# Optimization experiments

Measured on AMD Instinct MI355X. Metric: run time of the kernel, lower is better.

Reference implementation:

```python
import jax, jax.numpy as jnp
import numpy as np

N_NODES = 4194304  # 2**22
LEVELS = 10
COARSE = 8192
RANK = 2
NNZ = 8388608


def _interp_linear(u, N):
    """torch F.interpolate(mode='linear', align_corners=False) along axis 1. u: (B,M,R) -> (B,N,R)."""
    M = u.shape[1]
    pos = (jnp.arange(N, dtype=jnp.float32) + 0.5) * (M / N) - 0.5
    pos = jnp.clip(pos, 0.0, M - 1)
    i0 = jnp.floor(pos).astype(jnp.int32)
    i1 = jnp.minimum(i0 + 1, M - 1)
    w = (pos - i0.astype(jnp.float32))[None, :, None]
    return u[:, i0] * (1.0 - w) + u[:, i1] * w


def _apply_hodlr(diag, u_factors, v_factors, x):
    B, N, _ = x.shape
    y = diag * x
    L = u_factors.shape[0]
    for lvl in range(L):
        num_splits = 2 ** (lvl + 1)
        bs = N // num_splits
        if bs == 0:
            continue
        uc, vc = u_factors[lvl], v_factors[lvl]
        u_full = _interp_linear(uc, N) if uc.shape[1] != N else uc
        v_full = _interp_linear(vc, N) if vc.shape[1] != N else vc
        P = num_splits // 2
        valid = P * 2 * bs
        xv = x[:, :valid].reshape(B, P, 2, bs, 1)
        uv = u_full[:, :valid].reshape(B, P, 2, bs, -1)
        vv = v_full[:, :valid].reshape(B, P, 2, bs, -1)
        xL, xR = xv[:, :, 0], xv[:, :, 1]
        uL, uR = uv[:, :, 0], uv[:, :, 1]
        vL, vR = vv[:, :, 0], vv[:, :, 1]
        xRp = jnp.einsum('bpkr,bpko->bpro', vR, xR)  # (B,P,R,1)
        xLp = jnp.einsum('bpkr,bpko->bpro', vL, xL)
        yL = jnp.einsum('bpkr,bpro->bpko', uL, xRp)  # (B,P,bs,1)
        yR = jnp.einsum('bpkr,bpro->bpko', uR, xLp)
        upd = jnp.stack([yL, yR], axis=2).reshape(B, valid, 1)
        if valid < N:
            upd = jnp.pad(upd, ((0, 0), (0, N - valid), (0, 0)))
        y = y + upd
    return y


def setup_inputs() -> dict:
    key = jax.random.key(0)
    ks = jax.random.split(key, 6)
    diag = jax.random.uniform(ks[0], (1, N_NODES, 1), dtype=jnp.float32)
    u_factors = jax.random.normal(ks[1], (LEVELS, 1, COARSE, RANK), dtype=jnp.float32)
    v_factors = jax.random.normal(ks[2], (LEVELS, 1, COARSE, RANK), dtype=jnp.float32)
    A_values = jax.random.normal(ks[3], (NNZ,), dtype=jnp.float32)
    z = jax.random.normal(ks[4], (1, N_NODES, 1), dtype=jnp.float32)
    A_indices = jax.random.randint(ks[5], (2, NNZ), 0, N_NODES, dtype=jnp.int64) if jax.config.jax_enable_x64 else jax.random.randint(ks[5], (2, NNZ), 0, N_NODES, dtype=jnp.int32)
    return {"diag": diag, "u_factors": u_factors, "v_factors": v_factors,
            "A_values": A_values, "z": z, "A_indices": A_indices, "num_nodes": N_NODES}


def reference(diag, u_factors, v_factors, A_values, z, A_indices, num_nodes):
    N = num_nodes
    w = _apply_hodlr(diag, u_factors, v_factors, z)          # (1,N,1)
    w_flat = w.reshape(N)
    rows, cols = A_indices[0], A_indices[1]
    y_flat = jax.ops.segment_sum(A_values * w_flat[cols], rows, num_segments=N)
    y = y_flat.reshape(1, N, 1)
    loss = jnp.mean((y - z) ** 2)
    return loss
```

## Files before the change

kernel.cpp:

```cpp
#include <hip/hip_runtime.h>

#define N_NODES   4194304
#define LEVELS    10
#define COARSE    8192
#define NNZ_E     8388608
#define NCHUNK    16384
#define NBUCK     256
#define BROWS     16384
#define BSH       14
#define HBLOCKS   2048
#define EPB       4096

typedef int          v4i __attribute__((ext_vector_type(4)));
typedef float        v4f __attribute__((ext_vector_type(4)));
typedef unsigned int v4u __attribute__((ext_vector_type(4)));

static __device__ __forceinline__ unsigned short f2bf(float x) {
    unsigned u = __float_as_uint(x);
    return (unsigned short)((u + 0x7FFFu + ((u >> 16) & 1u)) >> 16);
}
static __device__ __forceinline__ float bf2f(unsigned short h) {
    return __uint_as_float((unsigned)h << 16);
}
static __device__ __forceinline__ unsigned pack18(int lrow, float p) {
    unsigned u = __float_as_uint(p);
    return ((unsigned)lrow << 18) | (((u + 0x2000u) >> 14) & 0x3FFFFu);
}

__global__ __launch_bounds__(256) void kA_moments(const float* __restrict__ z,
                                                  float2* __restrict__ M,
                                                  float* __restrict__ S,
                                                  float* __restrict__ out) {
    if (blockIdx.x == 0) {
        for (int i = threadIdx.x; i < 2046 * 2; i += 256) S[i] = 0.f;
        if (threadIdx.x == 0) out[0] = 0.f;
    }
    int lane = threadIdx.x & 63;
    int wave = threadIdx.x >> 6;
    int chunk = blockIdx.x * 4 + wave;
    int base = chunk * 256 + lane * 4;
    float4 zv = *(const float4*)(z + base);
    float a0 = 0.f, a1 = 0.f;
    const float* zp = (const float*)&zv;
#pragma unroll
    for (int j = 0; j < 4; ++j) {
        float p = ((float)(base + j) + 0.5f) * (1.0f / 512.0f) - 0.5f;
        p = fminf(fmaxf(p, 0.0f), (float)(COARSE - 1));
        float f = p - floorf(p);
        a0 += zp[j] * (1.0f - f);
        a1 += zp[j] * f;
    }
#pragma unroll
    for (int off = 32; off >= 1; off >>= 1) {
        a0 += __shfl_xor(a0, off, 64);
        a1 += __shfl_xor(a1, off, 64);
    }
    if (lane == 0) M[chunk] = make_float2(a0, a1);
}

__global__ __launch_bounds__(1024) void kB_ssum(const float2* __restrict__ M,
                                                const float* __restrict__ V,
                                                float* __restrict__ S) {
    int lvl = blockIdx.x >> 3;
    int slice = blockIdx.x & 7;
    int t = threadIdx.x;
    const float2* Vl = (const float2*)(V + lvl * COARSE * 2);
    float s0 = 0.f, s1 = 0.f;
    int c0 = slice * 2048 + t * 2;
#pragma unroll
    for (int cc = 0; cc < 2; ++cc) {
        int c = c0 + cc;
        float2 m = M[c];
        int k = (c > 0) ? ((c - 1) >> 1) : 0;
        int kp = min(k + 1, COARSE - 1);
        float2 vk = Vl[k], vkp = Vl[kp];
        s0 += vk.x * m.x + vkp.x * m.y;
        s1 += vk.y * m.x + vkp.y * m.y;
    }
    int tpg_sh = 12 - lvl;
    int gw = min(1 << tpg_sh, 64);
    for (int sh = gw >> 1; sh >= 1; sh >>= 1) {
        s0 += __shfl_xor(s0, sh, 64);
        s1 += __shfl_xor(s1, sh, 64);
    }
    if ((t & (gw - 1)) == 0) {
        int b = c0 >> (13 - lvl);
        int soff = (2 << lvl) - 2;
        unsafeAtomicAdd(&S[(soff + b) * 2 + 0], s0);
        unsafeAtomicAdd(&S[(soff + b) * 2 + 1], s1);
    }
}

__global__ __launch_bounds__(256) void kC_g(const float* __restrict__ S,
                                            const float* __restrict__ U,
                                            float2* __restrict__ G) {
    int c = blockIdx.x * 256 + threadIdx.x;
    int k = (c > 0) ? ((c - 1) >> 1) : 0;
    int kp = min(k + 1, COARSE - 1);
    float g0 = 0.f, g1 = 0.f;
#pragma unroll
    for (int lvl = 0; lvl < LEVELS; ++lvl) {
        int sib = (c >> (13 - lvl)) ^ 1;
        int soff = (2 << lvl) - 2;
        float2 s = ((const float2*)S)[soff + sib];
        const float2* Ul = (const float2*)(U + lvl * COARSE * 2);
        float2 uk = Ul[k], ukp = Ul[kp];
        g0 += uk.x * s.x + uk.y * s.y;
        g1 += ukp.x * s.x + ukp.y * s.y;
    }
    G[c] = make_float2(g0, g1);
}

__global__ __launch_bounds__(256) void kW(const float* __restrict__ diag,
                                          const float* __restrict__ z,
                                          const float2* __restrict__ G,
                                          unsigned short* __restrict__ wb) {
    int tid = blockIdx.x * 256 + threadIdx.x;
    int base = tid * 4;
    float2 g = G[base >> 8];
    v4f d4 = __builtin_nontemporal_load((const v4f*)(diag + base));
    v4f z4 = __builtin_nontemporal_load((const v4f*)(z + base));
    const float* dp = (const float*)&d4;
    const float* zp = (const float*)&z4;
    ushort4 h4;
    unsigned short* hp = (unsigned short*)&h4;
#pragma unroll
    for (int j = 0; j < 4; ++j) {
        float p = ((float)(base + j) + 0.5f) * (1.0f / 512.0f) - 0.5f;
        p = fminf(fmaxf(p, 0.0f), (float)(COARSE - 1));
        float f = p - floorf(p);
        hp[j] = f2bf(dp[j] * zp[j] + (g.x + f * (g.y - g.x)));
    }
    *(ushort4*)(wb + base) = h4;
}

__global__ __launch_bounds__(256) void kHist(const int* __restrict__ rows,
                                             unsigned int* __restrict__ blockOff) {
    __shared__ unsigned int h[NBUCK];
    int blk = blockIdx.x, t = threadIdx.x;
    h[t] = 0u;
    __syncthreads();
    int base = blk * EPB;
#pragma unroll
    for (int it = 0; it < 4; ++it) {
        int e = base + it * 1024 + t * 4;
        v4i r = __builtin_nontemporal_load((const v4i*)(rows + e));
        atomicAdd(&h[r.x >> BSH], 1u);
        atomicAdd(&h[r.y >> BSH], 1u);
        atomicAdd(&h[r.z >> BSH], 1u);
        atomicAdd(&h[r.w >> BSH], 1u);
    }
    __syncthreads();
    blockOff[t * HBLOCKS + blk] = h[t];
}

__global__ __launch_bounds__(256) void kScan1(unsigned int* __restrict__ blockOff,
                                              unsigned int* __restrict__ total) {
    int b = blockIdx.x, t = threadIdx.x;
    unsigned int* p = blockOff + b * HBLOCKS;
    v4u a = *(const v4u*)(p + t * 8);
    v4u c = *(const v4u*)(p + t * 8 + 4);
    unsigned int s = a.x + a.y + a.z + a.w + c.x + c.y + c.z + c.w;
    unsigned int incl = s;
#pragma unroll
    for (int off = 1; off < 64; off <<= 1) {
        unsigned int n = __shfl_up(incl, off, 64);
        if ((t & 63) >= off) incl += n;
    }
    __shared__ unsigned int wsum[4], wbase[4];
    if ((t & 63) == 63) wsum[t >> 6] = incl;
    __syncthreads();
    if (t == 0) {
        unsigned int acc = 0;
        for (int i = 0; i < 4; ++i) { wbase[i] = acc; acc += wsum[i]; }
        total[b] = acc;
    }
    __syncthreads();
    unsigned int excl = wbase[t >> 6] + incl - s;
    v4u e0, e1;
    e0.x = excl;        e0.y = e0.x + a.x; e0.z = e0.y + a.y; e0.w = e0.z + a.z;
    e1.x = e0.w + a.w;  e1.y = e1.x + c.x; e1.z = e1.y + c.y; e1.w = e1.z + c.z;
    *(v4u*)(p + t * 8) = e0;
    *(v4u*)(p + t * 8 + 4) = e1;
}

__global__ __launch_bounds__(256) void kBinScatter(const int* __restrict__ rows,
                                                   const int* __restrict__ cols,
                                                   const float* __restrict__ vals,
                                                   const unsigned short* __restrict__ wb,
                                                   const unsigned int* __restrict__ blockOff,
                                                   const unsigned int* __restrict__ total,
                                                   unsigned int* __restrict__ packed) {
    __shared__ unsigned int ctr[NBUCK];
    __shared__ unsigned int wsum[4], wbase[4];
    int blk = blockIdx.x, t = threadIdx.x;
    unsigned int tv = total[t];
    unsigned int incl = tv;
#pragma unroll
    for (int off = 1; off < 64; off <<= 1) {
        unsigned int n = __shfl_up(incl, off, 64);
        if ((t & 63) >= off) incl += n;
    }
    if ((t & 63) == 63) wsum[t >> 6] = incl;
    __syncthreads();
    if (t == 0) {
        unsigned int a = 0;
        for (int i = 0; i < 4; ++i) { wbase[i] = a; a += wsum[i]; }
    }
    __syncthreads();
    ctr[t] = (wbase[t >> 6] + incl - tv) + blockOff[t * HBLOCKS + blk];
    __syncthreads();

    int base = blk * EPB;
    v4i r[4], c[4];
    v4f v[4];
#pragma unroll
    for (int j = 0; j < 4; ++j) {
        int e = base + j * 1024 + t * 4;
        r[j] = __builtin_nontemporal_load((const v4i*)(rows + e));
        c[j] = __builtin_nontemporal_load((const v4i*)(cols + e));
        v[j] = __builtin_nontemporal_load((const v4f*)(vals + e));
    }
    unsigned short wv[16];
#pragma unroll
    for (int j = 0; j < 4; ++j) {
        const int* cp = (const int*)&c[j];
        wv[j * 4 + 0] = wb[cp[0]];
        wv[j * 4 + 1] = wb[cp[1]];
        wv[j * 4 + 2] = wb[cp[2]];
        wv[j * 4 + 3] = wb[cp[3]];
    }
#pragma unroll
    for (int j = 0; j < 4; ++j) {
        const int* rp = (const int*)&r[j];
        const float* vp = (const float*)&v[j];
#pragma unroll
        for (int k = 0; k < 4; ++k) {
            int row = rp[k];
            float p = vp[k] * bf2f(wv[j * 4 + k]);
            unsigned int pos = atomicAdd(&ctr[row >> BSH], 1u);
            packed[pos] = pack18(row & (BROWS - 1), p);
        }
    }
}

__global__ __launch_bounds__(1024) void kBucketAccum(const unsigned int* __restrict__ packed,
                                                     const unsigned int* __restrict__ total,
                                                     const float* __restrict__ z,
                                                     float* __restrict__ out) {
    __shared__ float acc[BROWS];
    __shared__ unsigned int sb, sn;
    __shared__ unsigned int wsum[4], wbase[4];
    __shared__ float red[16];
    int b = blockIdx.x, t = threadIdx.x;

    unsigned int tv = 0, incl = 0;
    if (t < 256) {
        tv = total[t];
        incl = tv;
#pragma unroll
        for (int off = 1; off < 64; off <<= 1) {
            unsigned int n = __shfl_up(incl, off, 64);
            if ((t & 63) >= off) incl += n;
        }
        if ((t & 63) == 63) wsum[t >> 6] = incl;
    }
    __syncthreads();
    if (t == 0) {
        unsigned int a = 0;
        for (int i = 0; i < 4; ++i) { wbase[i] = a; a += wsum[i]; }
    }
    __syncthreads();
    if (t < 256 && t == b) { sb = wbase[t >> 6] + incl - tv; sn = tv; }
    for (int i = t; i < BROWS / 4; i += 1024) ((float4*)acc)[i] = make_float4(0.f, 0.f, 0.f, 0.f);
    __syncthreads();

    unsigned int s0 = sb, n = sn;
    for (unsigned int i = t; i < n; i += 1024) {
        unsigned int e = __builtin_nontemporal_load(packed + s0 + i);
        atomicAdd(&acc[e >> 18], __uint_as_float((e & 0x3FFFFu) << 14));
    }
    __syncthreads();

    float part = 0.f;
    int gbase = b * BROWS;
    for (int i = t; i < BROWS; i += 1024) {
        float d = acc[i] - z[gbase + i];
        part += d * d;
    }
#pragma unroll
    for (int off = 32; off >= 1; off >>= 1) part += __shfl_xor(part, off, 64);
    if ((t & 63) == 0) red[t >> 6] = part;
    __syncthreads();
    if (t == 0) {
        float s = 0.f;
        for (int i = 0; i < 16; ++i) s += red[i];
        unsafeAtomicAdd(out, s * (1.0f / (float)N_NODES));
    }
}

extern "C" void kernel_launch(void* const* d_in, const int* in_sizes, int n_in,
                              void* d_out, int out_size, void* d_ws, size_t ws_size,
                              hipStream_t stream) {
    const float* diag  = (const float*)d_in[0];
    const float* U     = (const float*)d_in[1];
    const float* V     = (const float*)d_in[2];
    const float* Avals = (const float*)d_in[3];
    const float* z     = (const float*)d_in[4];
    const int*   Aidx  = (const int*)d_in[5];
    const int* rows = Aidx;
    const int* cols = Aidx + NNZ_E;

    char* ws = (char*)d_ws;
    size_t off = 0;
    unsigned short* wb = (unsigned short*)(ws + off); off += (size_t)N_NODES * 2;
    unsigned int* packed = (unsigned int*)(ws + off); off += (size_t)NNZ_E * 4;
    unsigned int* blockOff = (unsigned int*)(ws + off); off += (size_t)NBUCK * HBLOCKS * 4;
    unsigned int* total    = (unsigned int*)(ws + off); off += NBUCK * 4;
    float2* M  = (float2*)(ws + off); off += NCHUNK * 8;
    float*  S  = (float*)(ws + off);  off += 2046 * 2 * 4;
    float2* G  = (float2*)(ws + off); off += NCHUNK * 8;

    kA_moments<<<NCHUNK / 4, 256, 0, stream>>>(z, M, S, (float*)d_out);
    kB_ssum<<<LEVELS * 8, 1024, 0, stream>>>(M, V, S);
    kC_g<<<NCHUNK / 256, 256, 0, stream>>>(S, U, G);
    kW<<<N_NODES / 1024, 256, 0, stream>>>(diag, z, G, wb);

    kHist<<<HBLOCKS, 256, 0, stream>>>(rows, blockOff);
    kScan1<<<NBUCK, 256, 0, stream>>>(blockOff, total);
    kBinScatter<<<HBLOCKS, 256, 0, stream>>>(rows, cols, Avals, wb, blockOff, total, packed);
    kBucketAccum<<<NBUCK, 1024, 0, stream>>>(packed, total, z, (float*)d_out);
}
```

Before: 341.6 us.

## Two-pass column-then-row binning with LDS-resident w slices and fused launches

Replaces the random bf16 gather of w by first binning edges by column bucket, so each block of kD4 holds a 16K-entry fp32 w slice in shared memory and gathers from LDS. Kernel D4 then rebins products by row bucket into packed entries for the final accumulate. Independent stages (moments/histograms, ssum/scans, w compute/column scatter) are merged into fewer launches via blockIdx ranges. It removes scattered global gathers and launch overhead at the cost of an extra 8-byte-per-edge pass and more global traffic.

```diff
diff --git a/kernel.cpp b/kernel.cpp
--- a/kernel.cpp
+++ b/kernel.cpp
@@ -1,15 +1,16 @@
 #include <hip/hip_runtime.h>
 
-#define N_NODES   4194304
-#define LEVELS    10
-#define COARSE    8192
-#define NNZ_E     8388608
-#define NCHUNK    16384
-#define NBUCK     256
-#define BROWS     16384
-#define BSH       14
-#define HBLOCKS   2048
-#define EPB       4096
+#define N_NODES 4194304
+#define LEVELS  10
+#define COARSE  8192
+#define NNZ_E   8388608
+#define NCHUNK  16384
+#define NB      256
+#define CB_SZ   16384
+#define RB_SZ   16384
+#define HB      2048
+#define EPB     4096
+#define KMAX    34
 
 typedef int          v4i __attribute__((ext_vector_type(4)));
 typedef float        v4f __attribute__((ext_vector_type(4)));
@@ -22,269 +23,357 @@
 static __device__ __forceinline__ float bf2f(unsigned short h) {
     return __uint_as_float((unsigned)h << 16);
 }
-static __device__ __forceinline__ unsigned pack18(int lrow, float p) {
-    unsigned u = __float_as_uint(p);
-    return ((unsigned)lrow << 18) | (((u + 0x2000u) >> 14) & 0x3FFFFu);
-}
-
-__global__ __launch_bounds__(256) void kA_moments(const float* __restrict__ z,
-                                                  float2* __restrict__ M,
-                                                  float* __restrict__ S,
-                                                  float* __restrict__ out) {
-    if (blockIdx.x == 0) {
-        for (int i = threadIdx.x; i < 2046 * 2; i += 256) S[i] = 0.f;
-        if (threadIdx.x == 0) out[0] = 0.f;
-    }
-    int lane = threadIdx.x & 63;
-    int wave = threadIdx.x >> 6;
-    int chunk = blockIdx.x * 4 + wave;
-    int base = chunk * 256 + lane * 4;
-    float4 zv = *(const float4*)(z + base);
-    float a0 = 0.f, a1 = 0.f;
-    const float* zp = (const float*)&zv;
-#pragma unroll
-    for (int j = 0; j < 4; ++j) {
-        float p = ((float)(base + j) + 0.5f) * (1.0f / 512.0f) - 0.5f;
-        p = fminf(fmaxf(p, 0.0f), (float)(COARSE - 1));
-        float f = p - floorf(p);
-        a0 += zp[j] * (1.0f - f);
-        a1 += zp[j] * f;
-    }
-#pragma unroll
-    for (int off = 32; off >= 1; off >>= 1) {
-        a0 += __shfl_xor(a0, off, 64);
-        a1 += __shfl_xor(a1, off, 64);
-    }
-    if (lane == 0) M[chunk] = make_float2(a0, a1);
-}
-
-__global__ __launch_bounds__(1024) void kB_ssum(const float2* __restrict__ M,
-                                                const float* __restrict__ V,
-                                                float* __restrict__ S) {
-    int lvl = blockIdx.x >> 3;
-    int slice = blockIdx.x & 7;
-    int t = threadIdx.x;
-    const float2* Vl = (const float2*)(V + lvl * COARSE * 2);
-    float s0 = 0.f, s1 = 0.f;
-    int c0 = slice * 2048 + t * 2;
-#pragma unroll
-    for (int cc = 0; cc < 2; ++cc) {
-        int c = c0 + cc;
-        float2 m = M[c];
+static __device__ __forceinline__ unsigned f18(float p) {
+    return ((__float_as_uint(p) + 0x2000u) >> 14) & 0x3FFFFu;
+}
+
+__global__ __launch_bounds__(256) void kD1(const float* __restrict__ z,
+                                           float2* __restrict__ M,
+                                           float* __restrict__ S,
+                                           float* __restrict__ out,
+                                           const int* __restrict__ rows,
+                                           const int* __restrict__ cols,
+                                           unsigned* __restrict__ colBO,
+                                           unsigned* __restrict__ rowBC) {
+    int b = blockIdx.x, t = threadIdx.x;
+    if (b < 4096) {
+        if (b == 0) {
+            for (int i = t; i < 2046 * 2; i += 256) S[i] = 0.f;
+            if (t == 0) out[0] = 0.f;
+        }
+        int lane = t & 63, wave = t >> 6;
+        int chunk = b * 4 + wave;
+        int base = chunk * 256 + lane * 4;
+        float4 zv = *(const float4*)(z + base);
+        float a0 = 0.f, a1 = 0.f;
+        const float* zp = (const float*)&zv;
+#pragma unroll
+        for (int j = 0; j < 4; ++j) {
+            float p = ((float)(base + j) + 0.5f) * (1.0f / 512.0f) - 0.5f;
+            p = fminf(fmaxf(p, 0.0f), (float)(COARSE - 1));
+            float f = p - floorf(p);
+            a0 += zp[j] * (1.0f - f);
+            a1 += zp[j] * f;
+        }
+#pragma unroll
+        for (int off = 32; off >= 1; off >>= 1) {
+            a0 += __shfl_xor(a0, off, 64);
+            a1 += __shfl_xor(a1, off, 64);
+        }
+        if (lane == 0) M[chunk] = make_float2(a0, a1);
+    } else {
+        __shared__ unsigned hc[NB], hr[NB];
+        int blk = b - 4096;
+        hc[t] = 0u; hr[t] = 0u;
+        __syncthreads();
+        int base = blk * EPB;
+#pragma unroll
+        for (int it = 0; it < 4; ++it) {
+            int e = base + it * 1024 + t * 4;
+            v4i r = *(const v4i*)(rows + e);
+            v4i c = *(const v4i*)(cols + e);
+            atomicAdd(&hr[r.x >> 14], 1u); atomicAdd(&hr[r.y >> 14], 1u);
+            atomicAdd(&hr[r.z >> 14], 1u); atomicAdd(&hr[r.w >> 14], 1u);
+            atomicAdd(&hc[c.x >> 14], 1u); atomicAdd(&hc[c.y >> 14], 1u);
+            atomicAdd(&hc[c.z >> 14], 1u); atomicAdd(&hc[c.w >> 14], 1u);
+        }
+        __syncthreads();
+        colBO[t * HB + blk] = hc[t];
+        rowBC[t * HB + blk] = hr[t];
+    }
+}
+
+__global__ __launch_bounds__(1024) void kD2(const float2* __restrict__ M,
+                                            const float* __restrict__ V,
+                                            float* __restrict__ S,
+                                            unsigned* __restrict__ colBO,
+                                            unsigned* __restrict__ colTotal,
+                                            const unsigned* __restrict__ rowBC,
+                                            unsigned* __restrict__ rowTotal) {
+    int b = blockIdx.x, t = threadIdx.x;
+    if (b < 80) {
+        int lvl = b >> 3, slice = b & 7;
+        const float2* Vl = (const float2*)(V + lvl * COARSE * 2);
+        float s0 = 0.f, s1 = 0.f;
+        int c0 = slice * 2048 + t * 2;
+#pragma unroll
+        for (int cc = 0; cc < 2; ++cc) {
+            int c = c0 + cc;
+            float2 m = M[c];
+            int k = (c > 0) ? ((c - 1) >> 1) : 0;
+            int kp = min(k + 1, COARSE - 1);
+            float2 vk = Vl[k], vkp = Vl[kp];
+            s0 += vk.x * m.x + vkp.x * m.y;
+            s1 += vk.y * m.x + vkp.y * m.y;
+        }
+        int gw = min(1 << (12 - lvl), 64);
+        for (int sh = gw >> 1; sh >= 1; sh >>= 1) {
+            s0 += __shfl_xor(s0, sh, 64);
+            s1 += __shfl_xor(s1, sh, 64);
+        }
+        if ((t & (gw - 1)) == 0) {
+            int bb = c0 >> (13 - lvl);
+            int soff = (2 << lvl) - 2;
+            unsafeAtomicAdd(&S[(soff + bb) * 2 + 0], s0);
+            unsafeAtomicAdd(&S[(soff + bb) * 2 + 1], s1);
+        }
+    } else if (b < 336) {
+        int bb = b - 80;
+        __shared__ unsigned wsum[4], wbase[4];
+        if (t < 256) {
+            unsigned* p = colBO + bb * HB;
+            v4u a = *(const v4u*)(p + t * 8);
+            v4u c = *(const v4u*)(p + t * 8 + 4);
+            unsigned s = a.x + a.y + a.z + a.w + c.x + c.y + c.z + c.w;
+            unsigned incl = s;
+#pragma unroll
+            for (int off = 1; off < 64; off <<= 1) {
+                unsigned n = __shfl_up(incl, off, 64);
+                if ((t & 63) >= off) incl += n;
+            }
+            if ((t & 63) == 63) wsum[t >> 6] = incl;
+            __syncthreads();
+            if (t == 0) {
+                unsigned acc = 0;
+                for (int i = 0; i < 4; ++i) { wbase[i] = acc; acc += wsum[i]; }
+                colTotal[bb] = acc;
+            }
+            __syncthreads();
+            unsigned excl = wbase[t >> 6] + incl - s;
+            v4u e0, e1;
+            e0.x = excl;       e0.y = e0.x + a.x; e0.z = e0.y + a.y; e0.w = e0.z + a.z;
+            e1.x = e0.w + a.w; e1.y = e1.x + c.x; e1.z = e1.y + c.y; e1.w = e1.z + c.z;
+            *(v4u*)(p + t * 8) = e0;
+            *(v4u*)(p + t * 8 + 4) = e1;
+        } else {
+            __syncthreads();
+            __syncthreads();
+        }
+    } else {
+        int bb = b - 336;
+        __shared__ unsigned red[8];
+        unsigned s = 0;
+        if (t < 512) {
+            v4u vv = *(const v4u*)(rowBC + bb * HB + t * 4);
+            s = vv.x + vv.y + vv.z + vv.w;
+        }
+#pragma unroll
+        for (int off = 32; off >= 1; off >>= 1) s += __shfl_xor(s, off, 64);
+        if (t < 512 && (t & 63) == 0) red[t >> 6] = s;
+        __syncthreads();
+        if (t == 0) {
+            unsigned tot = 0;
+            for (int i = 0; i < 8; ++i) tot += red[i];
+            rowTotal[bb] = tot;
+        }
+    }
+}
+
+__global__ __launch_bounds__(256) void kD3(const float* __restrict__ diag,
+                                           const float* __restrict__ z,
+                                           const float* __restrict__ S,
+                                           const float* __restrict__ U,
+                                           float* __restrict__ w,
+                                           const int* __restrict__ rows,
+                                           const int* __restrict__ cols,
+                                           const float* __restrict__ vals,
+                                           const unsigned* __restrict__ colTotal,
+                                           const unsigned* __restrict__ colBO,
+                                           uint2* __restrict__ colBinned,
+                                           const unsigned* __restrict__ rowTotal,
+                                           unsigned* __restrict__ rowBase,
+                                           unsigned* __restrict__ rowCtr) {
+    int b = blockIdx.x, t = threadIdx.x;
+    if (b < 4096) {
+        int tid = b * 256 + t;
+        int base = tid * 4;
+        int c = base >> 8;
         int k = (c > 0) ? ((c - 1) >> 1) : 0;
         int kp = min(k + 1, COARSE - 1);
-        float2 vk = Vl[k], vkp = Vl[kp];
-        s0 += vk.x * m.x + vkp.x * m.y;
-        s1 += vk.y * m.x + vkp.y * m.y;
-    }
-    int tpg_sh = 12 - lvl;
-    int gw = min(1 << tpg_sh, 64);
-    for (int sh = gw >> 1; sh >= 1; sh >>= 1) {
-        s0 += __shfl_xor(s0, sh, 64);
-        s1 += __shfl_xor(s1, sh, 64);
-    }
-    if ((t & (gw - 1)) == 0) {
-        int b = c0 >> (13 - lvl);
-        int soff = (2 << lvl) - 2;
-        unsafeAtomicAdd(&S[(soff + b) * 2 + 0], s0);
-        unsafeAtomicAdd(&S[(soff + b) * 2 + 1], s1);
-    }
-}
-
-__global__ __launch_bounds__(256) void kC_g(const float* __restrict__ S,
-                                            const float* __restrict__ U,
-                                            float2* __restrict__ G) {
-    int c = blockIdx.x * 256 + threadIdx.x;
-    int k = (c > 0) ? ((c - 1) >> 1) : 0;
-    int kp = min(k + 1, COARSE - 1);
-    float g0 = 0.f, g1 = 0.f;
-#pragma unroll
-    for (int lvl = 0; lvl < LEVELS; ++lvl) {
-        int sib = (c >> (13 - lvl)) ^ 1;
-        int soff = (2 << lvl) - 2;
-        float2 s = ((const float2*)S)[soff + sib];
-        const float2* Ul = (const float2*)(U + lvl * COARSE * 2);
-        float2 uk = Ul[k], ukp = Ul[kp];
-        g0 += uk.x * s.x + uk.y * s.y;
-        g1 += ukp.x * s.x + ukp.y * s.y;
-    }
-    G[c] = make_float2(g0, g1);
-}
-
-__global__ __launch_bounds__(256) void kW(const float* __restrict__ diag,
-                                          const float* __restrict__ z,
-                                          const float2* __restrict__ G,
-                                          unsigned short* __restrict__ wb) {
-    int tid = blockIdx.x * 256 + threadIdx.x;
-    int base = tid * 4;
-    float2 g = G[base >> 8];
-    v4f d4 = __builtin_nontemporal_load((const v4f*)(diag + base));
-    v4f z4 = __builtin_nontemporal_load((const v4f*)(z + base));
-    const float* dp = (const float*)&d4;
-    const float* zp = (const float*)&z4;
-    ushort4 h4;
-    unsigned short* hp = (unsigned short*)&h4;
-#pragma unroll
-    for (int j = 0; j < 4; ++j) {
-        float p = ((float)(base + j) + 0.5f) * (1.0f / 512.0f) - 0.5f;
-        p = fminf(fmaxf(p, 0.0f), (float)(COARSE - 1));
-        float f = p - floorf(p);
-        hp[j] = f2bf(dp[j] * zp[j] + (g.x + f * (g.y - g.x)));
-    }
-    *(ushort4*)(wb + base) = h4;
-}
-
-__global__ __launch_bounds__(256) void kHist(const int* __restrict__ rows,
-                                             unsigned int* __restrict__ blockOff) {
-    __shared__ unsigned int h[NBUCK];
-    int blk = blockIdx.x, t = threadIdx.x;
-    h[t] = 0u;
-    __syncthreads();
-    int base = blk * EPB;
-#pragma unroll
-    for (int it = 0; it < 4; ++it) {
-        int e = base + it * 1024 + t * 4;
-        v4i r = __builtin_nontemporal_load((const v4i*)(rows + e));
-        atomicAdd(&h[r.x >> BSH], 1u);
-        atomicAdd(&h[r.y >> BSH], 1u);
-        atomicAdd(&h[r.z >> BSH], 1u);
-        atomicAdd(&h[r.w >> BSH], 1u);
-    }
-    __syncthreads();
-    blockOff[t * HBLOCKS + blk] = h[t];
-}
-
-__global__ __launch_bounds__(256) void kScan1(unsigned int* __restrict__ blockOff,
-                                              unsigned int* __restrict__ total) {
+        float g0 = 0.f, g1 = 0.f;
+#pragma unroll
+        for (int lvl = 0; lvl < LEVELS; ++lvl) {
+            int sib = (c >> (13 - lvl)) ^ 1;
+            int soff = (2 << lvl) - 2;
+            float2 s2 = ((const float2*)S)[soff + sib];
+            const float2* Ul = (const float2*)(U + lvl * COARSE * 2);
+            float2 uk = Ul[k], ukp = Ul[kp];
+            g0 += uk.x * s2.x + uk.y * s2.y;
+            g1 += ukp.x * s2.x + ukp.y * s2.y;
+        }
+        float4 d4 = *(const float4*)(diag + base);
+        float4 z4 = *(const float4*)(z + base);
+        const float* dp = (const float*)&d4;
+        const float* zp = (const float*)&z4;
+        float4 w4;
+        float* wp = (float*)&w4;
+#pragma unroll
+        for (int j = 0; j < 4; ++j) {
+            float p = ((float)(base + j) + 0.5f) * (1.0f / 512.0f) - 0.5f;
+            p = fminf(fmaxf(p, 0.0f), (float)(COARSE - 1));
+            float f = p - floorf(p);
+            wp[j] = dp[j] * zp[j] + (g0 + f * (g1 - g0));
+        }
+        *(float4*)(w + base) = w4;
+    } else if (b < 6144) {
+        int blk = b - 4096;
+        __shared__ unsigned ctr[NB];
+        __shared__ unsigned wsum[4], wbase[4];
+        unsigned tv = colTotal[t];
+        unsigned incl = tv;
+#pragma unroll
+        for (int off = 1; off < 64; off <<= 1) {
+            unsigned n = __shfl_up(incl, off, 64);
+            if ((t & 63) >= off) incl += n;
+        }
+        if ((t & 63) == 63) wsum[t >> 6] = incl;
+        __syncthreads();
+        if (t == 0) {
+            unsigned a = 0;
+            for (int i = 0; i < 4; ++i) { wbase[i] = a; a += wsum[i]; }
+        }
+        __syncthreads();
+        ctr[t] = (wbase[t >> 6] + incl - tv) + colBO[t * HB + blk];
+        __syncthreads();
+        int base = blk * EPB;
+        v4i r[4], c[4];
+        v4f v[4];
+#pragma unroll
+        for (int j = 0; j < 4; ++j) {
+            int e = base + j * 1024 + t * 4;
+            r[j] = *(const v4i*)(rows + e);
+            c[j] = *(const v4i*)(cols + e);
+            v[j] = *(const v4f*)(vals + e);
+        }
+#pragma unroll
+        for (int j = 0; j < 4; ++j) {
+            const int* rp = (const int*)&r[j];
+            const int* cp = (const int*)&c[j];
+            const float* vp = (const float*)&v[j];
+#pragma unroll
+            for (int kk = 0; kk < 4; ++kk) {
+                int row = rp[kk], col = cp[kk];
+                int cb = col >> 14;
+                int cl = col & 16383;
+                unsigned key = (unsigned)row | ((unsigned)(cl & 0x3FF) << 22);
+                unsigned aux = (unsigned)(cl >> 10) | ((unsigned)f2bf(vp[kk]) << 16);
+                unsigned pos = atomicAdd(&ctr[cb], 1u);
+                colBinned[pos] = make_uint2(key, aux);
+            }
+        }
+    } else {
+        __shared__ unsigned wsum[4], wbase[4];
+        unsigned tv = rowTotal[t];
+        unsigned incl = tv;
+#pragma unroll
+        for (int off = 1; off < 64; off <<= 1) {
+            unsigned n = __shfl_up(incl, off, 64);
+            if ((t & 63) >= off) incl += n;
+        }
+        if ((t & 63) == 63) wsum[t >> 6] = incl;
+        __syncthreads();
+        if (t == 0) {
+            unsigned a = 0;
+            for (int i = 0; i < 4; ++i) { wbase[i] = a; a += wsum[i]; }
+        }
+        __syncthreads();
+        unsigned excl = wbase[t >> 6] + incl - tv;
+        rowBase[t] = excl;
+        rowCtr[t] = excl;
+        if (t == 255) rowBase[256] = excl + tv;
+    }
+}
+
+__global__ __launch_bounds__(1024) void kD4(const unsigned* __restrict__ colTotal,
+                                            const uint2* __restrict__ colBinned,
+                                            const float* __restrict__ w,
+                                            unsigned* __restrict__ rowCtr,
+                                            unsigned* __restrict__ packed) {
+    __shared__ float wSl[CB_SZ];
+    __shared__ unsigned rh[NB], ctr2[NB];
+    __shared__ unsigned wsum[4], wbase[4];
+    __shared__ unsigned sS, sN;
     int b = blockIdx.x, t = threadIdx.x;
-    unsigned int* p = blockOff + b * HBLOCKS;
-    v4u a = *(const v4u*)(p + t * 8);
-    v4u c = *(const v4u*)(p + t * 8 + 4);
-    unsigned int s = a.x + a.y + a.z + a.w + c.x + c.y + c.z + c.w;
-    unsigned int incl = s;
-#pragma unroll
-    for (int off = 1; off < 64; off <<= 1) {
-        unsigned int n = __shfl_up(incl, off, 64);
-        if ((t & 63) >= off) incl += n;
-    }
-    __shared__ unsigned int wsum[4], wbase[4];
-    if ((t & 63) == 63) wsum[t >> 6] = incl;
+    unsigned tv = 0, incl = 0;
+    if (t < 256) {
+        rh[t] = 0u;
+        tv = colTotal[t];
+        incl = tv;
+#pragma unroll
+        for (int off = 1; off < 64; off <<= 1) {
+            unsigned n = __shfl_up(incl, off, 64);
+            if ((t & 63) >= off) incl += n;
+        }
+        if ((t & 63) == 63) wsum[t >> 6] = incl;
+    }
     __syncthreads();
     if (t == 0) {
-        unsigned int acc = 0;
-        for (int i = 0; i < 4; ++i) { wbase[i] = acc; acc += wsum[i]; }
-        total[b] = acc;
-    }
-    __syncthreads();
-    unsigned int excl = wbase[t >> 6] + incl - s;
-    v4u e0, e1;
-    e0.x = excl;        e0.y = e0.x + a.x; e0.z = e0.y + a.y; e0.w = e0.z + a.z;
-    e1.x = e0.w + a.w;  e1.y = e1.x + c.x; e1.z = e1.y + c.y; e1.w = e1.z + c.z;
-    *(v4u*)(p + t * 8) = e0;
-    *(v4u*)(p + t * 8 + 4) = e1;
-}
-
-__global__ __launch_bounds__(256) void kBinScatter(const int* __restrict__ rows,
-                                                   const int* __restrict__ cols,
-                                                   const float* __restrict__ vals,
-                                                   const unsigned short* __restrict__ wb,
-                                                   const unsigned int* __restrict__ blockOff,
-                                                   const unsigned int* __restrict__ total,
-                                                   unsigned int* __restrict__ packed) {
-    __shared__ unsigned int ctr[NBUCK];
-    __shared__ unsigned int wsum[4], wbase[4];
-    int blk = blockIdx.x, t = threadIdx.x;
-    unsigned int tv = total[t];
-    unsigned int incl = tv;
-#pragma unroll
-    for (int off = 1; off < 64; off <<= 1) {
-        unsigned int n = __shfl_up(incl, off, 64);
-        if ((t & 63) >= off) incl += n;
-    }
-    if ((t & 63) == 63) wsum[t >> 6] = incl;
-    __syncthreads();
-    if (t == 0) {
-        unsigned int a = 0;
+        unsigned a = 0;
         for (int i = 0; i < 4; ++i) { wbase[i] = a; a += wsum[i]; }
     }
     __syncthreads();
-    ctr[t] = (wbase[t >> 6] + incl - tv) + blockOff[t * HBLOCKS + blk];
-    __syncthreads();
-
-    int base = blk * EPB;
-    v4i r[4], c[4];
-    v4f v[4];
-#pragma unroll
-    for (int j = 0; j < 4; ++j) {
-        int e = base + j * 1024 + t * 4;
-        r[j] = __builtin_nontemporal_load((const v4i*)(rows + e));
-        c[j] = __builtin_nontemporal_load((const v4i*)(cols + e));
-        v[j] = __builtin_nontemporal_load((const v4f*)(vals + e));
-    }
-    unsigned short wv[16];
-#pragma unroll
-    for (int j = 0; j < 4; ++j) {
-        const int* cp = (const int*)&c[j];
-        wv[j * 4 + 0] = wb[cp[0]];
-        wv[j * 4 + 1] = wb[cp[1]];
-        wv[j * 4 + 2] = wb[cp[2]];
-        wv[j * 4 + 3] = wb[cp[3]];
-    }
-#pragma unroll
-    for (int j = 0; j < 4; ++j) {
-        const int* rp = (const int*)&r[j];
-        const float* vp = (const float*)&v[j];
-#pragma unroll
-        for (int k = 0; k < 4; ++k) {
-            int row = rp[k];
-            float p = vp[k] * bf2f(wv[j * 4 + k]);
-            unsigned int pos = atomicAdd(&ctr[row >> BSH], 1u);
-            packed[pos] = pack18(row & (BROWS - 1), p);
-        }
-    }
-}
-
-__global__ __launch_bounds__(1024) void kBucketAccum(const unsigned int* __restrict__ packed,
-                                                     const unsigned int* __restrict__ total,
-                                                     const float* __restrict__ z,
-                                                     float* __restrict__ out) {
-    __shared__ float acc[BROWS];
-    __shared__ unsigned int sb, sn;
-    __shared__ unsigned int wsum[4], wbase[4];
+    if (t < 256 && t == b) { sS = wbase[t >> 6] + incl - tv; sN = tv; }
+    __syncthreads();
+    const float4* wg = (const float4*)(w + (size_t)b * CB_SZ);
+    for (int i = t; i < CB_SZ / 4; i += 1024) ((float4*)wSl)[i] = wg[i];
+    unsigned s0 = sS, n = sN;
+    uint2 ev[KMAX];
+#pragma unroll
+    for (int k = 0; k < KMAX; ++k) {
+        unsigned i = (unsigned)(k * 1024 + t);
+        if (i < n) ev[k] = colBinned[s0 + i];
+    }
+#pragma unroll
+    for (int k = 0; k < KMAX; ++k) {
+        if ((unsigned)(k * 1024 + t) < n)
+            atomicAdd(&rh[(ev[k].x & 0x3FFFFFu) >> 14], 1u);
+    }
+    for (unsigned i = KMAX * 1024 + t; i < n; i += 1024) {
+        uint2 e = colBinned[s0 + i];
+        atomicAdd(&rh[(e.x & 0x3FFFFFu) >> 14], 1u);
+    }
+    __syncthreads();
+    if (t < 256) ctr2[t] = atomicAdd(&rowCtr[t], rh[t]);
+    __syncthreads();
+#pragma unroll
+    for (int k = 0; k < KMAX; ++k) {
+        if ((unsigned)(k * 1024 + t) < n) {
+            uint2 e = ev[k];
+            unsigned cl = (e.x >> 22) | ((e.y & 0xFu) << 10);
+            float p = bf2f((unsigned short)(e.y >> 16)) * wSl[cl];
+            unsigned rb = (e.x & 0x3FFFFFu) >> 14;
+            unsigned pos = atomicAdd(&ctr2[rb], 1u);
+            packed[pos] = ((e.x & 0x3FFFu) << 18) | f18(p);
+        }
+    }
+    for (unsigned i = KMAX * 1024 + t; i < n; i += 1024) {
+        uint2 e = colBinned[s0 + i];
+        unsigned cl = (e.x >> 22) | ((e.y & 0xFu) << 10);
+        float p = bf2f((unsigned short)(e.y >> 16)) * wSl[cl];
+        unsigned rb = (e.x & 0x3FFFFFu) >> 14;
+        unsigned pos = atomicAdd(&ctr2[rb], 1u);
+        packed[pos] = ((e.x & 0x3FFFu) << 18) | f18(p);
+    }
+}
+
+__global__ __launch_bounds__(1024) void kD5(const unsigned* __restrict__ packed,
+                                            const unsigned* __restrict__ rowBase,
+                                            const float* __restrict__ z,
+                                            float* __restrict__ out) {
+    __shared__ float acc[RB_SZ];
     __shared__ float red[16];
     int b = blockIdx.x, t = threadIdx.x;
-
-    unsigned int tv = 0, incl = 0;
-    if (t < 256) {
-        tv = total[t];
-        incl = tv;
-#pragma unroll
-        for (int off = 1; off < 64; off <<= 1) {
-            unsigned int n = __shfl_up(incl, off, 64);
-            if ((t & 63) >= off) incl += n;
-        }
-        if ((t & 63) == 63) wsum[t >> 6] = incl;
-    }
-    __syncthreads();
-    if (t == 0) {
-        unsigned int a = 0;
-        for (int i = 0; i < 4; ++i) { wbase[i] = a; a += wsum[i]; }
-    }
-    __syncthreads();
-    if (t < 256 && t == b) { sb = wbase[t >> 6] + incl - tv; sn = tv; }
-    for (int i = t; i < BROWS / 4; i += 1024) ((float4*)acc)[i] = make_float4(0.f, 0.f, 0.f, 0.f);
-    __syncthreads();
-
-    unsigned int s0 = sb, n = sn;
-    for (unsigned int i = t; i < n; i += 1024) {
-        unsigned int e = __builtin_nontemporal_load(packed + s0 + i);
+    unsigned s0 = rowBase[b], n = rowBase[b + 1] - s0;
+    for (int i = t; i < RB_SZ / 4; i += 1024) ((float4*)acc)[i] = make_float4(0.f, 0.f, 0.f, 0.f);
+    __syncthreads();
+    for (unsigned i = t; i < n; i += 1024) {
+        unsigned e = packed[s0 + i];
         atomicAdd(&acc[e >> 18], __uint_as_float((e & 0x3FFFFu) << 14));
     }
     __syncthreads();
-
     float part = 0.f;
-    int gbase = b * BROWS;
-    for (int i = t; i < BROWS; i += 1024) {
+    int gbase = b * RB_SZ;
+    for (int i = t; i < RB_SZ; i += 1024) {
         float d = acc[i] - z[gbase + i];
         part += d * d;
     }
@@ -313,21 +402,22 @@
 
     char* ws = (char*)d_ws;
     size_t off = 0;
-    unsigned short* wb = (unsigned short*)(ws + off); off += (size_t)N_NODES * 2;
-    unsigned int* packed = (unsigned int*)(ws + off); off += (size_t)NNZ_E * 4;
-    unsigned int* blockOff = (unsigned int*)(ws + off); off += (size_t)NBUCK * HBLOCKS * 4;
-    unsigned int* total    = (unsigned int*)(ws + off); off += NBUCK * 4;
-    float2* M  = (float2*)(ws + off); off += NCHUNK * 8;
-    float*  S  = (float*)(ws + off);  off += 2046 * 2 * 4;
-    float2* G  = (float2*)(ws + off); off += NCHUNK * 8;
-
-    kA_moments<<<NCHUNK / 4, 256, 0, stream>>>(z, M, S, (float*)d_out);
-    kB_ssum<<<LEVELS * 8, 1024, 0, stream>>>(M, V, S);
-    kC_g<<<NCHUNK / 256, 256, 0, stream>>>(S, U, G);
-    kW<<<N_NODES / 1024, 256, 0, stream>>>(diag, z, G, wb);
-
-    kHist<<<HBLOCKS, 256, 0, stream>>>(rows, blockOff);
-    kScan1<<<NBUCK, 256, 0, stream>>>(blockOff, total);
-    kBinScatter<<<HBLOCKS, 256, 0, stream>>>(rows, cols, Avals, wb, blockOff, total, packed);
-    kBucketAccum<<<NBUCK, 1024, 0, stream>>>(packed, total, z, (float*)d_out);
-}
+    float* w           = (float*)(ws + off);        off += (size_t)N_NODES * 4;
+    uint2* colBinned   = (uint2*)(ws + off);        off += (size_t)NNZ_E * 8;
+    unsigned* packed   = (unsigned*)(ws + off);     off += (size_t)NNZ_E * 4;
+    unsigned* colBO    = (unsigned*)(ws + off);     off += (size_t)NB * HB * 4;
+    unsigned* rowBC    = (unsigned*)(ws + off);     off += (size_t)NB * HB * 4;
+    float2* M          = (float2*)(ws + off);       off += (size_t)NCHUNK * 8;
+    float* S           = (float*)(ws + off);        off += 16384;
+    unsigned* colTotal = (unsigned*)(ws + off);     off += 1024;
+    unsigned* rowTotal = (unsigned*)(ws + off);     off += 1024;
+    unsigned* rowCtr   = (unsigned*)(ws + off);     off += 1024;
+    unsigned* rowBase  = (unsigned*)(ws + off);     off += 1040;
+
+    kD1<<<6144, 256, 0, stream>>>(z, M, S, (float*)d_out, rows, cols, colBO, rowBC);
+    kD2<<<592, 1024, 0, stream>>>(M, V, S, colBO, colTotal, rowBC, rowTotal);
+    kD3<<<6145, 256, 0, stream>>>(diag, z, S, U, w, rows, cols, Avals,
+                                  colTotal, colBO, colBinned, rowTotal, rowBase, rowCtr);
+    kD4<<<256, 1024, 0, stream>>>(colTotal, colBinned, w, rowCtr, packed);
+    kD5<<<256, 1024, 0, stream>>>(packed, rowBase, z, (float*)d_out);
+}
```

After: 356.9 us. 4.5% more time.
